# Kernel tuning notes

Measured on AMD Instinct MI355X. Metric: run time of the kernel, lower is better.

## Reference

```python
import jax, jax.numpy as jnp
import numpy as np
from jax import lax

B, S, D, N_ORDER, K = 8, 4096, 256, 2, 3
G = N_ORDER + 1  # groups in HyenaProjection
EPS_FILT = 1e-8


def setup_inputs() -> dict:
    key = jax.random.key(0)
    ks = jax.random.split(key, 8)
    sc = 0.02
    # positions: per-row arange with trailing -1 padding (one contiguous read per row)
    vl = jnp.where(jnp.arange(B) % 2 == 0, S, (3 * S) // 4)
    pos = jnp.where(jnp.arange(S, dtype=jnp.int32)[None, :] < vl[:, None],
                    jnp.arange(S, dtype=jnp.int32)[None, :], -1)
    return {
        "embeddings": jax.random.normal(ks[0], (B, S, D), jnp.float32),
        "positions": pos,
        "W_proj": jax.random.normal(ks[1], (D, G * D), jnp.float32) * sc,
        "conv_w": jax.random.normal(ks[2], (G * D, D, K), jnp.float32) * sc,
        "conv_b": jnp.zeros((G * D,), jnp.float32),
        "W1": jax.random.normal(ks[3], (D, D), jnp.float32) * sc,
        "b1": jnp.zeros((D,), jnp.float32),
        "ln_g": jnp.ones((D,), jnp.float32),
        "ln_b": jnp.zeros((D,), jnp.float32),
        "W2": jax.random.normal(ks[4], (D, N_ORDER * D), jnp.float32) * sc,
        "b2": jnp.zeros((N_ORDER * D,), jnp.float32),
        "ff_scale": jnp.ones((1, 1, N_ORDER * D), jnp.float32),
        "W_out": jax.random.normal(ks[5], (D, D), jnp.float32) * sc,
        "b_out": jnp.zeros((D,), jnp.float32),
    }


def adjust_positions(pos):
    pf = jnp.where(pos == -1, jnp.inf, pos.astype(jnp.float32))
    minp = pf.min(axis=-1, keepdims=True)
    adj = pos.astype(jnp.float32) - minp
    return jnp.where(pos == -1, -1.0, adj)


def rope_rotate(x, adj_pos):
    # compute_theta_vector + compute_rotation_angles + apply_dimensionwise_rotation
    d2 = x.shape[-1] // 2
    theta = 1.0 / (10000.0 ** (jnp.arange(d2, dtype=jnp.float32) / d2))
    ang = adj_pos[..., None] * theta  # (b, s, d/2)
    cos, sin = jnp.cos(ang), jnp.sin(ang)
    x1, x2 = x[..., 0::2], x[..., 1::2]
    r1 = x1 * cos - x2 * sin
    r2 = x1 * sin + x2 * cos
    return jnp.stack([r1, r2], axis=-1).reshape(x.shape)


def feed_forward(x, W1, b1, ln_g, ln_b, W2, b2, ff_scale):
    h = x @ W1 + b1
    mu = h.mean(-1, keepdims=True)
    var = ((h - mu) ** 2).mean(-1, keepdims=True)
    h = (h - mu) / jnp.sqrt(var + 1e-5) * ln_g + ln_b
    h = jax.nn.gelu(h, approximate=False)
    return (h @ W2 + b2) * ff_scale


def fft_long_conv(x, f, mask):
    # x, f: (b, d, s); 2L zero-padded circular conv == linear conv; torch norm='forward' pair => /n net
    L = x.shape[-1]
    n = 2 * L
    y = jnp.fft.irfft(jnp.fft.rfft(x, n=n) * jnp.fft.rfft(f, n=n), n=n)[..., :L] / n
    return y * mask[:, None, :]


def reference(embeddings, positions, W_proj, conv_w, conv_b, W1, b1, ln_g, ln_b, W2, b2, ff_scale, W_out, b_out):
    mask = (positions != -1).astype(embeddings.dtype)  # (b, s)

    # HyenaProjection: linear -> grouped short conv -> mask -> split into G streams
    z = jnp.einsum('bsd,de->bes', embeddings, W_proj)  # (b, G*d, s)
    z = lax.conv_general_dilated(z, conv_w, (1,), [(K // 2, K // 2)],
                                 dimension_numbers=('NCH', 'OIH', 'NCH'),
                                 feature_group_count=G)
    z = (z + conv_b[None, :, None]) * mask[:, None, :]
    zs = jnp.split(z, G, axis=1)  # G tensors of (b, d, s)

    # HyenaFilter: RoPE -> FFN -> reshape (b, n, d, s) -> L1 normalize over d
    t = rope_rotate(embeddings, adjust_positions(positions))
    h_hat = feed_forward(t, W1, b1, ln_g, ln_b, W2, b2, ff_scale)  # (b, s, n*d)
    h_hat = h_hat.reshape(h_hat.shape[0], h_hat.shape[1], N_ORDER, D).transpose(0, 2, 3, 1)
    h_hat = h_hat / (jnp.sum(jnp.abs(h_hat), axis=2, keepdims=True) + EPS_FILT)

    # Hyena recurrence with FFT long convolutions
    v = zs[-1]
    for i in range(N_ORDER):
        v = zs[i] * fft_long_conv(v, h_hat[:, i], mask)

    out = jnp.einsum('bds,de->bse', v, W_out) + b_out
    return out * mask[..., None]  # reassemble leaves padded positions zero
```

## Files before the change

### kernel.cpp

```cpp
#include <hip/hip_runtime.h>
#include <cstdint>

#define S_LEN 4096
#define D_DIM 256

#define OFF_MINP 0
#define OFF_WPT  16
#define OFF_WTH  (OFF_WPT + 768*256)
#define OFF_WTL  (OFF_WTH + 294912)
#define OFF_C    (OFF_WTL + 294912)
#define OFF_HH   (OFF_C + 8*768*4096)
#define OFF_V    (OFF_HH + 8*2*256*4096)
#define OFF_U    (OFF_V + 8*256*4096)


typedef __attribute__((ext_vector_type(8))) short short8;
typedef __attribute__((ext_vector_type(4))) float f32x4;

__device__ __forceinline__ unsigned int f2bf(float x) {
    union { float f; unsigned int u; } v; v.f = x;
    unsigned int r = v.u + 0x7fffu + ((v.u >> 16) & 1u);
    return r >> 16;
}
__device__ __forceinline__ float bf2f(unsigned int h) {
    union { unsigned int u; float f; } v; v.u = h << 16; return v.f;
}

__global__ __launch_bounds__(256) void k_minpos(const int* __restrict__ pos, float* __restrict__ minp)
{
    const int b = blockIdx.x;
    const int tid = threadIdx.x;
    int mn = 0x7fffffff;
    const int* p = pos + (size_t)b * S_LEN;
    for (int s = tid; s < S_LEN; s += 256) {
        const int v = p[s];
        if (v != -1) mn = min(mn, v);
    }
    __shared__ int red[256];
    red[tid] = mn;
    __syncthreads();
    for (int st = 128; st > 0; st >>= 1) {
        if (tid < st) red[tid] = min(red[tid], red[tid + st]);
        __syncthreads();
    }
    if (tid == 0) minp[b] = (float)red[0];
}

__global__ __launch_bounds__(256) void k_wpt(const float* __restrict__ Wp, float* __restrict__ WpT)
{
    __shared__ float t[32][33];
    const int e0 = blockIdx.x * 32;
    const int d0 = blockIdx.y * 32;
    const int lx = threadIdx.x & 31, ly = threadIdx.x >> 5;
#pragma unroll
    for (int q = 0; q < 4; ++q)
        t[ly + 8*q][lx] = Wp[(size_t)(d0 + ly + 8*q) * 768 + e0 + lx];
    __syncthreads();
#pragma unroll
    for (int q = 0; q < 4; ++q)
        WpT[(size_t)(e0 + ly + 8*q) * 256 + d0 + lx] = t[lx][ly + 8*q];
}

__global__ __launch_bounds__(256) void k_tsplit(const float* __restrict__ W, const int K, const int N,
                                                unsigned short* __restrict__ oh, unsigned short* __restrict__ ol)
{
    __shared__ float t[32][33];
    const int n0 = blockIdx.x * 32;
    const int k0 = blockIdx.y * 32;
    const int lx = threadIdx.x & 31, ly = threadIdx.x >> 5;
#pragma unroll
    for (int q = 0; q < 4; ++q)
        t[ly + 8*q][lx] = W[(size_t)(k0 + ly + 8*q) * N + n0 + lx];
    __syncthreads();
#pragma unroll
    for (int q = 0; q < 4; ++q) {
        const float v = t[lx][ly + 8*q];
        const unsigned int h = f2bf(v);
        oh[(size_t)(n0 + ly + 8*q) * K + k0 + lx] = (unsigned short)h;
        ol[(size_t)(n0 + ly + 8*q) * K + k0 + lx] = (unsigned short)f2bf(v - bf2f(h));
    }
}

__global__ __launch_bounds__(256) void k_weff(const float* __restrict__ WpT, const float* __restrict__ cw,
                                              unsigned short* __restrict__ wth, unsigned short* __restrict__ wtl)
{
    const int o = blockIdx.x;
    const int d = threadIdx.x;
    const int g = o >> 8;
    __shared__ float cwrow[768];
    for (int i = threadIdx.x; i < 768; i += 256) cwrow[i] = cw[(size_t)o * 768 + i];
    __syncthreads();
    float a0 = 0.f, a1 = 0.f, a2 = 0.f;
    const float* wb = WpT + (size_t)(g * 256) * 256 + d;
#pragma unroll 4
    for (int i = 0; i < 256; ++i) {
        const float wv = wb[(size_t)i * 256];
        a0 += wv * cwrow[i*3+0];
        a1 += wv * cwrow[i*3+1];
        a2 += wv * cwrow[i*3+2];
    }
    const float av[3] = {a0, a1, a2};
#pragma unroll
    for (int t = 0; t < 3; ++t) {
        const unsigned int hb = f2bf(av[t]);
        const unsigned int lb = f2bf(av[t] - bf2f(hb));
        wth[(size_t)o * 768 + t * 256 + d] = (unsigned short)hb;
        wtl[(size_t)o * 768 + t * 256 + d] = (unsigned short)lb;
    }
}

#define CG_LDA 40
__global__ __launch_bounds__(256, 3) void k_convgemm(
    const float* __restrict__ emb, const int* __restrict__ pos,
    const unsigned short* __restrict__ wth, const unsigned short* __restrict__ wtl,
    const float* __restrict__ convb, float* __restrict__ c)
{
    const int b  = blockIdx.z;
    const int o0 = blockIdx.y * 128;
    const int s0 = blockIdx.x * 128;
    const int tid  = threadIdx.x;
    const int wave = tid >> 6, lane = tid & 63;
    const int m16  = lane & 15, quad = lane >> 4;

    __shared__ __align__(16) unsigned short As[130 * CG_LDA];
    __shared__ __align__(16) unsigned short Bh[128 * CG_LDA];
    __shared__ __align__(16) unsigned short Bl[128 * CG_LDA];

    const int rA = tid >> 1;
    const int cA = (tid & 1) * 16;
    const int srowA = s0 + rA - 1;
    const bool vA = (srowA >= 0 && srowA < S_LEN);
    const float* embA = emb + ((size_t)b * S_LEN + (vA ? srowA : 0)) * D_DIM + cA;
    const int rT = 128 + (tid >> 3);
    const int cT = (tid & 7) * 4;
    const int srowT = s0 + rT - 1;
    const bool vT = (tid < 16) && (srowT >= 0 && srowT < S_LEN);
    const float* embT = emb + ((size_t)b * S_LEN + ((tid < 16 && vT) ? srowT : 0)) * D_DIM + cT;

    const int rB0 = tid >> 2,        gB0 = (tid & 3) * 8;
    const int rB1 = 64 + (tid >> 2), gB1 = gB0;

    float4 apf[4]; float4 apfT;
    uint4 bph0, bpl0, bph1, bpl1;

#pragma unroll
    for (int q = 0; q < 4; ++q) apf[q] = vA ? *(const float4*)(embA + q * 4) : make_float4(0.f,0.f,0.f,0.f);
    apfT = vT ? *(const float4*)(embT) : make_float4(0.f,0.f,0.f,0.f);
    {
        const size_t gi0 = (size_t)(o0 + rB0) * 768 + gB0;
        const size_t gi1 = (size_t)(o0 + rB1) * 768 + gB1;
        bph0 = *(const uint4*)(wth + gi0); bpl0 = *(const uint4*)(wtl + gi0);
        bph1 = *(const uint4*)(wth + gi1); bpl1 = *(const uint4*)(wtl + gi1);
    }

    f32x4 acc[2][8];
#pragma unroll
    for (int mt = 0; mt < 2; ++mt)
#pragma unroll
        for (int nt = 0; nt < 8; ++nt)
#pragma unroll
            for (int e = 0; e < 4; ++e) acc[mt][nt][e] = 0.f;

    for (int c8 = 0; c8 < 8; ++c8) {
        for (int t = 0; t < 3; ++t) {
            __syncthreads();
            if (t == 0) {
#pragma unroll
                for (int q = 0; q < 4; ++q) {
                    const float4 v = apf[q];
                    uint2 hp;
                    hp.x = f2bf(v.x) | (f2bf(v.y) << 16);
                    hp.y = f2bf(v.z) | (f2bf(v.w) << 16);
                    *(uint2*)&As[rA * CG_LDA + cA + q * 4] = hp;
                }
                if (tid < 16) {
                    const float4 v = apfT;
                    uint2 hp;
                    hp.x = f2bf(v.x) | (f2bf(v.y) << 16);
                    hp.y = f2bf(v.z) | (f2bf(v.w) << 16);
                    *(uint2*)&As[rT * CG_LDA + cT] = hp;
                }
                if (c8 < 7) {
                    const int base = (c8 + 1) * 32;
#pragma unroll
                    for (int q = 0; q < 4; ++q) apf[q] = vA ? *(const float4*)(embA + base + q * 4) : make_float4(0.f,0.f,0.f,0.f);
                    apfT = vT ? *(const float4*)(embT + base) : make_float4(0.f,0.f,0.f,0.f);
                }
            }
            *(uint4*)&Bh[rB0 * CG_LDA + gB0] = bph0;
            *(uint4*)&Bl[rB0 * CG_LDA + gB0] = bpl0;
            *(uint4*)&Bh[rB1 * CG_LDA + gB1] = bph1;
            *(uint4*)&Bl[rB1 * CG_LDA + gB1] = bpl1;
            if (!(c8 == 7 && t == 2)) {
                const int t2  = (t == 2) ? 0 : (t + 1);
                const int c82 = c8 + (t == 2);
                const int kbase = t2 * 256 + c82 * 32;
                const size_t gi0 = (size_t)(o0 + rB0) * 768 + kbase + gB0;
                const size_t gi1 = (size_t)(o0 + rB1) * 768 + kbase + gB1;
                bph0 = *(const uint4*)(wth + gi0); bpl0 = *(const uint4*)(wtl + gi0);
                bph1 = *(const uint4*)(wth + gi1); bpl1 = *(const uint4*)(wtl + gi1);
            }
            __syncthreads();
            short8 ah[2];
#pragma unroll
            for (int mt = 0; mt < 2; ++mt) {
                const int ar = (wave * 32 + mt * 16 + m16 + t) * CG_LDA + quad * 8;
                ah[mt] = *(const short8*)&As[ar];
            }
#pragma unroll
            for (int nt = 0; nt < 8; ++nt) {
                const int br = (nt * 16 + m16) * CG_LDA + quad * 8;
                const short8 bh = *(const short8*)&Bh[br];
                const short8 bl = *(const short8*)&Bl[br];
#pragma unroll
                for (int mt = 0; mt < 2; ++mt) {
                    acc[mt][nt] = __builtin_amdgcn_mfma_f32_16x16x32_bf16(ah[mt], bh, acc[mt][nt], 0, 0, 0);
                    acc[mt][nt] = __builtin_amdgcn_mfma_f32_16x16x32_bf16(ah[mt], bl, acc[mt][nt], 0, 0, 0);
                }
            }
        }
    }
    __syncthreads();

    float msk[2][4];
#pragma unroll
    for (int mt = 0; mt < 2; ++mt) {
        const int s = s0 + wave * 32 + mt * 16 + quad * 4;
        const int4 p4 = *(const int4*)(pos + (size_t)b * S_LEN + s);
        msk[mt][0] = (p4.x != -1) ? 1.f : 0.f;
        msk[mt][1] = (p4.y != -1) ? 1.f : 0.f;
        msk[mt][2] = (p4.z != -1) ? 1.f : 0.f;
        msk[mt][3] = (p4.w != -1) ? 1.f : 0.f;
    }
#pragma unroll
    for (int nt = 0; nt < 8; ++nt) {
        const int o = o0 + nt * 16 + m16;
        const float cb = convb[o];
#pragma unroll
        for (int mt = 0; mt < 2; ++mt) {
            const int s = s0 + wave * 32 + mt * 16 + quad * 4;
            float4 r;
            r.x = (acc[mt][nt][0] + cb) * msk[mt][0];
            r.y = (acc[mt][nt][1] + cb) * msk[mt][1];
            r.z = (acc[mt][nt][2] + cb) * msk[mt][2];
            r.w = (acc[mt][nt][3] + cb) * msk[mt][3];
            *(float4*)(c + ((size_t)(b * 768 + o)) * S_LEN + s) = r;
        }
    }
}

#define FF_LDA 264
#define FF_LDB 136
__global__ __launch_bounds__(256, 2) void k_ff(
    const float* __restrict__ emb, const int* __restrict__ pos, const float* __restrict__ minp,
    const unsigned short* __restrict__ w1th, const unsigned short* __restrict__ w1tl,
    const float* __restrict__ b1,
    const float* __restrict__ lng, const float* __restrict__ lnb,
    const unsigned short* __restrict__ w2th, const unsigned short* __restrict__ w2tl,
    const float* __restrict__ b2, const float* __restrict__ ffs, float* __restrict__ hh)
{
    const int b   = blockIdx.y;
    const int s0  = blockIdx.x * 64;
    const int tid = threadIdx.x;
    const int wave = tid >> 6, lane = tid & 63;
    const int m16  = lane & 15, quad = lane >> 4;

    __shared__ __align__(16) unsigned short Th[64 * FF_LDA];
    __shared__ __align__(16) unsigned short Bsh[16 * FF_LDB];
    __shared__ __align__(16) unsigned short Bsl[16 * FF_LDB];
    __shared__ float th_s[128];

    if (tid < 128) th_s[tid] = expf(-(float)tid * 0.07195578415606394f);
    __syncthreads();

    {
        const int r    = tid >> 2;
        const int col0 = (tid & 3) * 64;
        const int s    = s0 + r;
        const int p    = pos[(size_t)b * S_LEN + s];
        const float adj = (p == -1) ? -1.f : ((float)p - minp[b]);
        const float* ep = emb + ((size_t)b * S_LEN + s) * D_DIM;
#pragma unroll
        for (int p8 = 0; p8 < 8; ++p8) {
            const int cbase = col0 + p8 * 8;
            const float4 va = *(const float4*)(ep + cbase);
            const float4 vb4 = *(const float4*)(ep + cbase + 4);
            const float x[8] = {va.x, va.y, va.z, va.w, vb4.x, vb4.y, vb4.z, vb4.w};
            unsigned int uh[4];
#pragma unroll
            for (int jj = 0; jj < 4; ++jj) {
                const int j = (cbase >> 1) + jj;
                const float theta = th_s[j];
                float sn, cs;
                sincosf(adj * theta, &sn, &cs);
                const float x1 = x[2*jj], x2 = x[2*jj+1];
                const float r1 = x1 * cs - x2 * sn;
                const float r2 = x1 * sn + x2 * cs;
                uh[jj] = f2bf(r1) | (f2bf(r2) << 16);
            }
            uint4 wh;
            wh.x = uh[0]; wh.y = uh[1]; wh.z = uh[2]; wh.w = uh[3];
            *(uint4*)&Th[r * FF_LDA + cbase] = wh;
        }
    }
    __syncthreads();

    const int rowA  = wave * 16 + m16;
    const int strow = tid >> 4;
    const int stks  = (tid & 15) * 8;

    f32x4 acc1[16];
#pragma unroll
    for (int nt = 0; nt < 16; ++nt)
#pragma unroll
        for (int e = 0; e < 4; ++e) acc1[nt][e] = 0.f;

    uint4 pfh, pfl;
    {
        const size_t gi = (size_t)strow * 256 + stks;
        pfh = *(const uint4*)(w1th + gi);
        pfl = *(const uint4*)(w1tl + gi);
    }
    for (int kh = 0; kh < 2; ++kh) {
        short8 a1h[4];
#pragma unroll
        for (int c4 = 0; c4 < 4; ++c4) {
            const int ar = rowA * FF_LDA + kh * 128 + c4 * 32 + quad * 8;
            a1h[c4] = *(const short8*)&Th[ar];
        }
#pragma unroll
        for (int nt = 0; nt < 16; ++nt) {
            __syncthreads();
            *(uint4*)&Bsh[strow * FF_LDB + stks] = pfh;
            *(uint4*)&Bsl[strow * FF_LDB + stks] = pfl;
            if (!(kh == 1 && nt == 15)) {
                const int nt2 = (nt + 1) & 15;
                const int kh2 = kh + (nt == 15);
                const size_t gi = (size_t)(nt2 * 16 + strow) * 256 + kh2 * 128 + stks;
                pfh = *(const uint4*)(w1th + gi);
                pfl = *(const uint4*)(w1tl + gi);
            }
            __syncthreads();
#pragma unroll
            for (int c4 = 0; c4 < 4; ++c4) {
                const int br = m16 * FF_LDB + c4 * 32 + quad * 8;
                const short8 bh = *(const short8*)&Bsh[br];
                const short8 bl = *(const short8*)&Bsl[br];
                acc1[nt] = __builtin_amdgcn_mfma_f32_16x16x32_bf16(a1h[c4], bh, acc1[nt], 0, 0, 0);
                acc1[nt] = __builtin_amdgcn_mfma_f32_16x16x32_bf16(a1h[c4], bl, acc1[nt], 0, 0, 0);
            }
        }
    }

    float sume[4] = {0.f, 0.f, 0.f, 0.f}, sumq[4] = {0.f, 0.f, 0.f, 0.f};
#pragma unroll
    for (int nt = 0; nt < 16; ++nt) {
        const float bb = b1[nt * 16 + m16];
#pragma unroll
        for (int e = 0; e < 4; ++e) {
            const float v = acc1[nt][e] + bb;
            acc1[nt][e] = v;
            sume[e] += v;
            sumq[e] += v * v;
        }
    }
#pragma unroll
    for (int e = 0; e < 4; ++e) {
#pragma unroll
        for (int off = 1; off < 16; off <<= 1) {
            sume[e] += __shfl_xor(sume[e], off, 64);
            sumq[e] += __shfl_xor(sumq[e], off, 64);
        }
    }
    float mu[4], rs[4];
#pragma unroll
    for (int e = 0; e < 4; ++e) {
        mu[e] = sume[e] * (1.f / 256.f);
        const float var = sumq[e] * (1.f / 256.f) - mu[e] * mu[e];
        rs[e] = rsqrtf(var + 1e-5f);
    }

    {
        const size_t gi = (size_t)strow * 256 + stks;
        pfh = *(const uint4*)(w2th + gi);
        pfl = *(const uint4*)(w2tl + gi);
    }

    __syncthreads();
#pragma unroll
    for (int nt = 0; nt < 16; ++nt) {
        const int col = nt * 16 + m16;
        const float g  = lng[col];
        const float be = lnb[col];
#pragma unroll
        for (int e = 0; e < 4; ++e) {
            const float h  = (acc1[nt][e] - mu[e]) * rs[e] * g + be;
            const float hg = 0.5f * h * (1.f + erff(h * 0.7071067811865475f));
            const int li = (wave * 16 + quad * 4 + e) * FF_LDA + col;
            Th[li] = (unsigned short)f2bf(hg);
        }
    }
    __syncthreads();

    f32x4 acc2[32];
#pragma unroll
    for (int nt = 0; nt < 32; ++nt)
#pragma unroll
        for (int e = 0; e < 4; ++e) acc2[nt][e] = 0.f;

    for (int kh = 0; kh < 2; ++kh) {
        short8 a2h[4];
#pragma unroll
        for (int c4 = 0; c4 < 4; ++c4) {
            const int ar = rowA * FF_LDA + kh * 128 + c4 * 32 + quad * 8;
            a2h[c4] = *(const short8*)&Th[ar];
        }
#pragma unroll
        for (int nt = 0; nt < 32; ++nt) {
            __syncthreads();
            *(uint4*)&Bsh[strow * FF_LDB + stks] = pfh;
            *(uint4*)&Bsl[strow * FF_LDB + stks] = pfl;
            if (!(kh == 1 && nt == 31)) {
                const int nt2 = (nt + 1) & 31;
                const int kh2 = kh + (nt == 31);
                const size_t gi = (size_t)(nt2 * 16 + strow) * 256 + kh2 * 128 + stks;
                pfh = *(const uint4*)(w2th + gi);
                pfl = *(const uint4*)(w2tl + gi);
            }
            __syncthreads();
#pragma unroll
            for (int c4 = 0; c4 < 4; ++c4) {
                const int br = m16 * FF_LDB + c4 * 32 + quad * 8;
                const short8 bh = *(const short8*)&Bsh[br];
                const short8 bl = *(const short8*)&Bsl[br];
                acc2[nt] = __builtin_amdgcn_mfma_f32_16x16x32_bf16(a2h[c4], bh, acc2[nt], 0, 0, 0);
                acc2[nt] = __builtin_amdgcn_mfma_f32_16x16x32_bf16(a2h[c4], bl, acc2[nt], 0, 0, 0);
            }
        }
    }

    float sm[2][4] = {{0.f,0.f,0.f,0.f},{0.f,0.f,0.f,0.f}};
#pragma unroll
    for (int nt = 0; nt < 32; ++nt) {
        const int col = nt * 16 + m16;
        const float bb = b2[col];
        const float fs = ffs[col];
#pragma unroll
        for (int e = 0; e < 4; ++e) {
            const float v = (acc2[nt][e] + bb) * fs;
            acc2[nt][e] = v;
            sm[nt >> 4][e] += fabsf(v);
        }
    }
#pragma unroll
    for (int i = 0; i < 2; ++i)
#pragma unroll
        for (int e = 0; e < 4; ++e) {
#pragma unroll
            for (int off = 1; off < 16; off <<= 1)
                sm[i][e] += __shfl_xor(sm[i][e], off, 64);
        }
#pragma unroll
    for (int nt = 0; nt < 32; ++nt) {
        const int i = nt >> 4;
        const int d = (nt & 15) * 16 + m16;
        float4 o4;
        o4.x = acc2[nt][0] / (sm[i][0] + 1e-8f);
        o4.y = acc2[nt][1] / (sm[i][1] + 1e-8f);
        o4.z = acc2[nt][2] / (sm[i][2] + 1e-8f);
        o4.w = acc2[nt][3] / (sm[i][3] + 1e-8f);
        *(float4*)(hh + ((size_t)((b * 2 + i) * 256 + d)) * S_LEN + s0 + wave * 16 + quad * 4) = o4;
    }
}

#define XS_PAD   960
#define XS_ELEMS 5056
#define FRX_WORDS 4160
__device__ __forceinline__ int xsw(int blk) { return blk ^ ((blk >> 3) & 7); }

#define CONV_ACCUM_LOOP(ACC)                                                         \
    for (int i = 0; i < 32; ++i) {                                                   \
        const int r = 2 * i + wid;                                                   \
        const int ea_r = eA_base - 64 * r;                                           \
        short8 afr[4][2];                                                            \
        _Pragma("unroll")                                                            \
        for (int mt = 0; mt < 4; ++mt)                                               \
            _Pragma("unroll")                                                        \
            for (int kc = 0; kc < 2; ++kc) {                                         \
                const int e = ea_r - 16 * mt + 32 * kc;                              \
                union { unsigned int u[4]; short8 s; } cvt;                          \
                cvt.u[0] = frx[e];                                                   \
                cvt.u[1] = frx[e + 2];                                               \
                cvt.u[2] = frx[e + 4];                                               \
                cvt.u[3] = frx[e + 6];                                               \
                afr[mt][kc] = cvt.s;                                                 \
            }                                                                        \
        const int ptmin = r >> 4;                                                    \
        const int ob_r = oB_base - 64 * r;                                           \
        _Pragma("unroll")                                                            \
        for (int pt = 0; pt < 4; ++pt) {                                             \
            if (pt >= ptmin) {                                                       \
                const int o0 = ob_r + 1024 * pt;                                     \
                const short8 bfr0 = *(const short8*)(xs + xsw(o0 >> 3) * 8);         \
                const short8 bfr1 = *(const short8*)(xs + xsw((o0 + 32) >> 3) * 8);  \
                _Pragma("unroll")                                                    \
                for (int mt = 0; mt < 4; ++mt) {                                     \
                    ACC[mt][pt] = __builtin_amdgcn_mfma_f32_16x16x32_bf16(afr[mt][0], bfr0, ACC[mt][pt], 0, 0, 0); \
                    ACC[mt][pt] = __builtin_amdgcn_mfma_f32_16x16x32_bf16(afr[mt][1], bfr1, ACC[mt][pt], 0, 0, 0); \
                }                                                                    \
            }                                                                        \
        }                                                                            \
    }

__global__ __launch_bounds__(128) void k_conv2x(
    const float* __restrict__ cbuf, const float* __restrict__ hh,
    float* __restrict__ outb)
{
    const int d = blockIdx.x;
    const int b = blockIdx.y;
    const int tid  = threadIdx.x;
    const int lane = tid & 63;
    const int wid  = tid >> 6;
    const float* xp  = cbuf + ((size_t)(b * 768 + 512 + d)) * S_LEN;
    const float* fp0 = hh   + ((size_t)((b * 2 + 0) * 256 + d)) * S_LEN;
    const float* fp1 = hh   + ((size_t)((b * 2 + 1) * 256 + d)) * S_LEN;
    const float* zp0 = cbuf + ((size_t)(b * 768 +   0 + d)) * S_LEN;
    const float* zp1 = cbuf + ((size_t)(b * 768 + 256 + d)) * S_LEN;
    float* op = outb + ((size_t)(b * 256 + d)) * S_LEN;

    __shared__ __align__(16) unsigned short xs[XS_ELEMS];
    __shared__ __align__(16) unsigned int   frx[FRX_WORDS];

    float4 f1pf[8];
#pragma unroll
    for (int it = 0; it < 8; ++it)
        f1pf[it] = *(const float4*)(fp1 + (it * 128 + tid) * 4);

    {
        for (int blk = tid; blk < 120; blk += 128) {
            int4 z; z.x = 0; z.y = 0; z.z = 0; z.w = 0;
            *(int4*)(xs + xsw(blk) * 8) = z;
        }
#pragma unroll
        for (int it = 0; it < 4; ++it) {
            const int idx = it * 128 + tid;
            const int j = idx * 8;
            const float4 v0 = *(const float4*)(xp + j);
            const float4 v1 = *(const float4*)(xp + j + 4);
            int4 w;
            w.x = (int)(f2bf(v0.x) | (f2bf(v0.y) << 16));
            w.y = (int)(f2bf(v0.z) | (f2bf(v0.w) << 16));
            w.z = (int)(f2bf(v1.x) | (f2bf(v1.y) << 16));
            w.w = (int)(f2bf(v1.z) | (f2bf(v1.w) << 16));
            *(int4*)(xs + xsw(120 + idx) * 8) = w;
        }
    }
    {
        if (tid < 64) frx[4096 + tid] = 0u;
        if (tid == 0) frx[4095] = f2bf(fp0[0]);
#pragma unroll
        for (int it = 0; it < 8; ++it) {
            const int j = (it * 128 + tid) * 4;
            const float4 v = *(const float4*)(fp0 + j);
            const float f4 = (j + 4 < S_LEN) ? fp0[j + 4] : 0.f;
            frx[4094 - j] = f2bf(v.y) | (f2bf(v.x) << 16);
            frx[4093 - j] = f2bf(v.z) | (f2bf(v.y) << 16);
            frx[4092 - j] = f2bf(v.w) | (f2bf(v.z) << 16);
            if (j < 4092) frx[4091 - j] = f2bf(f4) | (f2bf(v.w) << 16);
        }
    }
    __syncthreads();

    const int m    = lane & 15;
    const int quad = lane >> 4;
    const int eA_base = 4095 - m + quad * 8;
    const int oB_base = XS_PAD + 64 * m + quad * 8;
    const float inv = 1.f / 8192.f;
    float* red = (float*)frx;

    f32x4 acc[4][4];
#pragma unroll
    for (int mt = 0; mt < 4; ++mt)
#pragma unroll
        for (int pt = 0; pt < 4; ++pt)
#pragma unroll
            for (int e = 0; e < 4; ++e) acc[mt][pt][e] = 0.f;

    CONV_ACCUM_LOOP(acc)

    __syncthreads();
    if (wid == 1) {
#pragma unroll
        for (int mt = 0; mt < 4; ++mt)
#pragma unroll
            for (int pt = 0; pt < 4; ++pt)
                *(f32x4*)&red[((mt * 4 + pt) * 64 + lane) * 4] = acc[mt][pt];
    }
    __syncthreads();
    if (wid == 0) {
#pragma unroll
        for (int mt = 0; mt < 4; ++mt)
#pragma unroll
            for (int pt = 0; pt < 4; ++pt) {
                const f32x4 po = *(const f32x4*)&red[((mt * 4 + pt) * 64 + lane) * 4];
                const int p  = 16 * pt + m;
                const int sv = 64 * p + 16 * mt + quad * 4;
                const float4 z4 = *(const float4*)(zp0 + sv);
                const float v0 = z4.x * (acc[mt][pt][0] + po[0]) * inv;
                const float v1 = z4.y * (acc[mt][pt][1] + po[1]) * inv;
                const float v2 = z4.z * (acc[mt][pt][2] + po[2]) * inv;
                const float v3 = z4.w * (acc[mt][pt][3] + po[3]) * inv;
                uint2 hp;
                hp.x = f2bf(v0) | (f2bf(v1) << 16);
                hp.y = f2bf(v2) | (f2bf(v3) << 16);
                *(uint2*)(xs + xsw(120 + (sv >> 3)) * 8 + (sv & 7)) = hp;
            }
    }
    __syncthreads();

    {
        if (tid < 64) frx[4096 + tid] = 0u;
        if (tid == 0) frx[4095] = f2bf(fp1[0]);
#pragma unroll
        for (int it = 0; it < 8; ++it) {
            const int j = (it * 128 + tid) * 4;
            const float4 v = f1pf[it];
            const float f4 = (j + 4 < S_LEN) ? fp1[j + 4] : 0.f;
            frx[4094 - j] = f2bf(v.y) | (f2bf(v.x) << 16);
            frx[4093 - j] = f2bf(v.z) | (f2bf(v.y) << 16);
            frx[4092 - j] = f2bf(v.w) | (f2bf(v.z) << 16);
            if (j < 4092) frx[4091 - j] = f2bf(f4) | (f2bf(v.w) << 16);
        }
    }
#pragma unroll
    for (int mt = 0; mt < 4; ++mt)
#pragma unroll
        for (int pt = 0; pt < 4; ++pt)
#pragma unroll
            for (int e = 0; e < 4; ++e) acc[mt][pt][e] = 0.f;
    __syncthreads();

    CONV_ACCUM_LOOP(acc)

    __syncthreads();
    if (wid == 1) {
#pragma unroll
        for (int mt = 0; mt < 4; ++mt)
#pragma unroll
            for (int pt = 0; pt < 4; ++pt)
                *(f32x4*)&red[((mt * 4 + pt) * 64 + lane) * 4] = acc[mt][pt];
    }
    __syncthreads();
    if (wid == 0) {
#pragma unroll
        for (int mt = 0; mt < 4; ++mt)
#pragma unroll
            for (int pt = 0; pt < 4; ++pt) {
                const f32x4 po = *(const f32x4*)&red[((mt * 4 + pt) * 64 + lane) * 4];
                const int p  = 16 * pt + m;
                const int sv = 64 * p + 16 * mt + quad * 4;
                const float4 z4 = *(const float4*)(zp1 + sv);
                float4 o4;
                o4.x = z4.x * (acc[mt][pt][0] + po[0]) * inv;
                o4.y = z4.y * (acc[mt][pt][1] + po[1]) * inv;
                o4.z = z4.z * (acc[mt][pt][2] + po[2]) * inv;
                o4.w = z4.w * (acc[mt][pt][3] + po[3]) * inv;
                *(float4*)(op + sv) = o4;
            }
    }
}

__global__ __launch_bounds__(256) void k_out(
    const float* __restrict__ v, const float* __restrict__ Wo,
    const float* __restrict__ bo, const int* __restrict__ pos,
    float* __restrict__ out)
{
    const int b   = blockIdx.y;
    const int s0  = blockIdx.x * 32;
    const int tid = threadIdx.x;
    __shared__ float vs[256 * 36];
    {
        const float4* src = (const float4*)(v + ((size_t)(b*256 + tid)) * S_LEN + s0);
#pragma unroll
        for (int q = 0; q < 8; ++q) {
            *(float4*)&vs[tid*36 + q*4] = src[q];
        }
    }
    __syncthreads();
    float acc[32];
#pragma unroll
    for (int r = 0; r < 32; ++r) acc[r] = 0.f;
    for (int dd = 0; dd < 256; ++dd) {
        const float w = Wo[(size_t)dd * 256 + tid];
        const float* vr = &vs[dd * 36];
#pragma unroll
        for (int q = 0; q < 8; ++q) {
            const float4 x4 = *(const float4*)&vr[q*4];
            acc[q*4+0] += x4.x * w;
            acc[q*4+1] += x4.y * w;
            acc[q*4+2] += x4.z * w;
            acc[q*4+3] += x4.w * w;
        }
    }
    const float bb = bo[tid];
#pragma unroll
    for (int r = 0; r < 32; ++r) {
        const int s = s0 + r;
        const float m = (pos[(size_t)b * S_LEN + s] != -1) ? 1.f : 0.f;
        out[((size_t)b * S_LEN + s) * 256 + tid] = (acc[r] + bb) * m;
    }
}

extern "C" void kernel_launch(void* const* d_in, const int* in_sizes, int n_in,
                              void* d_out, int out_size, void* d_ws, size_t ws_size,
                              hipStream_t stream) {
    const float* emb = (const float*)d_in[0];
    const int*   pos = (const int*)  d_in[1];
    const float* Wp  = (const float*)d_in[2];
    const float* cw  = (const float*)d_in[3];
    const float* cb  = (const float*)d_in[4];
    const float* W1  = (const float*)d_in[5];
    const float* b1  = (const float*)d_in[6];
    const float* lg  = (const float*)d_in[7];
    const float* lb  = (const float*)d_in[8];
    const float* W2  = (const float*)d_in[9];
    const float* b2  = (const float*)d_in[10];
    const float* ffs = (const float*)d_in[11];
    const float* Wo  = (const float*)d_in[12];
    const float* bo  = (const float*)d_in[13];

    float* ws   = (float*)d_ws;
    float* minp = ws + OFF_MINP;
    float* wpt  = ws + OFF_WPT;
    unsigned short* wth = (unsigned short*)(ws + OFF_WTH);
    unsigned short* wtl = (unsigned short*)(ws + OFF_WTL);
    float* c    = ws + OFF_C;
    float* hh   = ws + OFF_HH;
    float* vb   = ws + OFF_V;
    float* ub   = ws + OFF_U;

    unsigned short* w1th = (unsigned short*)vb;
    unsigned short* w1tl = w1th + 256 * 256;
    unsigned short* w2th = w1tl + 256 * 256;
    unsigned short* w2tl = w2th + 512 * 256;

    k_minpos<<<dim3(8), dim3(256), 0, stream>>>(pos, minp);
    k_wpt<<<dim3(24, 8), dim3(256), 0, stream>>>(Wp, wpt);
    k_weff<<<dim3(768), dim3(256), 0, stream>>>(wpt, cw, wth, wtl);
    k_tsplit<<<dim3(8, 8), dim3(256), 0, stream>>>(W1, 256, 256, w1th, w1tl);
    k_tsplit<<<dim3(16, 8), dim3(256), 0, stream>>>(W2, 256, 512, w2th, w2tl);
    k_convgemm<<<dim3(32, 6, 8), dim3(256), 0, stream>>>(emb, pos, wth, wtl, cb, c);
    k_ff<<<dim3(64, 8), dim3(256), 0, stream>>>(emb, pos, minp, w1th, w1tl, b1, lg, lb, w2th, w2tl, b2, ffs, hh);
    k_conv2x<<<dim3(256, 8), dim3(128), 0, stream>>>(c, hh, ub);
    k_out<<<dim3(128, 8), dim3(256), 0, stream>>>(ub, Wo, bo, pos, (float*)d_out);
}
```

Baseline: 484.0 us.

## Move output projection to bf16 split MFMA and widen conv filter LDS reads

```diff
diff --git a/kernel.cpp b/kernel.cpp
--- a/kernel.cpp
+++ b/kernel.cpp
@@ -488,11 +488,13 @@
             _Pragma("unroll")                                                        \
             for (int kc = 0; kc < 2; ++kc) {                                         \
                 const int e = ea_r - 16 * mt + 32 * kc;                              \
+                const uint2 d0 = frxd[e + 2];                                        \
+                const uint2 d1 = frxd[e + 6];                                        \
                 union { unsigned int u[4]; short8 s; } cvt;                          \
-                cvt.u[0] = frx[e];                                                   \
-                cvt.u[1] = frx[e + 2];                                               \
-                cvt.u[2] = frx[e + 4];                                               \
-                cvt.u[3] = frx[e + 6];                                               \
+                cvt.u[0] = d0.y;                                                     \
+                cvt.u[1] = d0.x;                                                     \
+                cvt.u[2] = d1.y;                                                     \
+                cvt.u[3] = d1.x;                                                     \
                 afr[mt][kc] = cvt.s;                                                 \
             }                                                                        \
         const int ptmin = r >> 4;                                                    \
@@ -512,6 +514,37 @@
         }                                                                            \
     }
 
+#define BUILD_FRXD(FPTR, VEXPR)                                                      \
+    {                                                                                \
+        _Pragma("unroll")                                                            \
+        for (int it = 0; it < 8; ++it) {                                             \
+            const int j = (it * 128 + tid) * 4;                                      \
+            const float4 v = (VEXPR);                                                \
+            const float4 g4 = (j + 4 < S_LEN) ? *(const float4*)((FPTR) + j + 4)     \
+                                              : make_float4(0.f,0.f,0.f,0.f);       \
+            const unsigned int w0 = f2bf(v.y)  | (f2bf(v.x)  << 16);                 \
+            const unsigned int w1 = f2bf(v.z)  | (f2bf(v.y)  << 16);                 \
+            const unsigned int w2 = f2bf(v.w)  | (f2bf(v.z)  << 16);                 \
+            const unsigned int w3 = f2bf(g4.x) | (f2bf(v.w)  << 16);                 \
+            const unsigned int w4 = f2bf(g4.y) | (f2bf(g4.x) << 16);                 \
+            const unsigned int w5 = f2bf(g4.z) | (f2bf(g4.y) << 16);                 \
+            frxd[4094 - j] = make_uint2(w0, w2);                                     \
+            frxd[4093 - j] = make_uint2(w1, w3);                                     \
+            frxd[4092 - j] = make_uint2(w2, w4);                                     \
+            if (j < 4092) frxd[4091 - j] = make_uint2(w3, w5);                       \
+        }                                                                            \
+        if (tid == 0) {                                                              \
+            const float4 v0 = *(const float4*)(FPTR);                                \
+            const unsigned int a95 = f2bf(v0.x);                                     \
+            const unsigned int w94 = f2bf(v0.y) | (f2bf(v0.x) << 16);                \
+            const unsigned int w93 = f2bf(v0.z) | (f2bf(v0.y) << 16);                \
+            frxd[4095] = make_uint2(a95, w93);                                       \
+            frxd[4096] = make_uint2(0u, w94);                                        \
+            frxd[4097] = make_uint2(0u, a95);                                        \
+        }                                                                            \
+        if (tid >= 2 && tid < 64) frxd[4096 + tid] = make_uint2(0u, 0u);             \
+    }
+
 __global__ __launch_bounds__(128) void k_conv2x(
     const float* __restrict__ cbuf, const float* __restrict__ hh,
     float* __restrict__ outb)
@@ -529,7 +562,7 @@
     float* op = outb + ((size_t)(b * 256 + d)) * S_LEN;
 
     __shared__ __align__(16) unsigned short xs[XS_ELEMS];
-    __shared__ __align__(16) unsigned int   frx[FRX_WORDS];
+    __shared__ __align__(16) uint2 frxd[FRX_WORDS];
 
     float4 f1pf[8];
 #pragma unroll
@@ -555,20 +588,7 @@
             *(int4*)(xs + xsw(120 + idx) * 8) = w;
         }
     }
-    {
-        if (tid < 64) frx[4096 + tid] = 0u;
-        if (tid == 0) frx[4095] = f2bf(fp0[0]);
-#pragma unroll
-        for (int it = 0; it < 8; ++it) {
-            const int j = (it * 128 + tid) * 4;
-            const float4 v = *(const float4*)(fp0 + j);
-            const float f4 = (j + 4 < S_LEN) ? fp0[j + 4] : 0.f;
-            frx[4094 - j] = f2bf(v.y) | (f2bf(v.x) << 16);
-            frx[4093 - j] = f2bf(v.z) | (f2bf(v.y) << 16);
-            frx[4092 - j] = f2bf(v.w) | (f2bf(v.z) << 16);
-            if (j < 4092) frx[4091 - j] = f2bf(f4) | (f2bf(v.w) << 16);
-        }
-    }
+    BUILD_FRXD(fp0, *(const float4*)(fp0 + j))
     __syncthreads();
 
     const int m    = lane & 15;
@@ -576,7 +596,7 @@
     const int eA_base = 4095 - m + quad * 8;
     const int oB_base = XS_PAD + 64 * m + quad * 8;
     const float inv = 1.f / 8192.f;
-    float* red = (float*)frx;
+    float* red = (float*)frxd;
 
     f32x4 acc[4][4];
 #pragma unroll
@@ -618,20 +638,7 @@
     }
     __syncthreads();
 
-    {
-        if (tid < 64) frx[4096 + tid] = 0u;
-        if (tid == 0) frx[4095] = f2bf(fp1[0]);
-#pragma unroll
-        for (int it = 0; it < 8; ++it) {
-            const int j = (it * 128 + tid) * 4;
-            const float4 v = f1pf[it];
-            const float f4 = (j + 4 < S_LEN) ? fp1[j + 4] : 0.f;
-            frx[4094 - j] = f2bf(v.y) | (f2bf(v.x) << 16);
-            frx[4093 - j] = f2bf(v.z) | (f2bf(v.y) << 16);
-            frx[4092 - j] = f2bf(v.w) | (f2bf(v.z) << 16);
-            if (j < 4092) frx[4091 - j] = f2bf(f4) | (f2bf(v.w) << 16);
-        }
-    }
+    BUILD_FRXD(fp1, f1pf[it])
 #pragma unroll
     for (int mt = 0; mt < 4; ++mt)
 #pragma unroll
@@ -670,44 +677,91 @@
     }
 }
 
-__global__ __launch_bounds__(256) void k_out(
-    const float* __restrict__ v, const float* __restrict__ Wo,
-    const float* __restrict__ bo, const int* __restrict__ pos,
-    float* __restrict__ out)
+__global__ __launch_bounds__(256, 2) void k_out(
+    const float* __restrict__ u, const unsigned short* __restrict__ woth,
+    const unsigned short* __restrict__ wotl, const float* __restrict__ bo,
+    const int* __restrict__ pos, float* __restrict__ out)
 {
     const int b   = blockIdx.y;
-    const int s0  = blockIdx.x * 32;
+    const int s0  = blockIdx.x * 64;
     const int tid = threadIdx.x;
-    __shared__ float vs[256 * 36];
+    const int wave = tid >> 6, lane = tid & 63;
+    const int m16  = lane & 15, quad = lane >> 4;
+
+    __shared__ __align__(16) unsigned short Bsh[16 * FF_LDB];
+    __shared__ __align__(16) unsigned short Bsl[16 * FF_LDB];
+
+    const int strow = tid >> 4;
+    const int stks  = (tid & 15) * 8;
+
+    const int sA = s0 + wave * 16 + m16;
+    const float* uA = u + (size_t)b * 256 * S_LEN + sA;
+
+    f32x4 acc[16];
+#pragma unroll
+    for (int nt = 0; nt < 16; ++nt)
+#pragma unroll
+        for (int e = 0; e < 4; ++e) acc[nt][e] = 0.f;
+
+    uint4 pfh, pfl;
     {
-        const float4* src = (const float4*)(v + ((size_t)(b*256 + tid)) * S_LEN + s0);
-#pragma unroll
-        for (int q = 0; q < 8; ++q) {
-            *(float4*)&vs[tid*36 + q*4] = src[q];
-        }
-    }
-    __syncthreads();
-    float acc[32];
-#pragma unroll
-    for (int r = 0; r < 32; ++r) acc[r] = 0.f;
-    for (int dd = 0; dd < 256; ++dd) {
-        const float w = Wo[(size_t)dd * 256 + tid];
-        const float* vr = &vs[dd * 36];
-#pragma unroll
-        for (int q = 0; q < 8; ++q) {
-            const float4 x4 = *(const float4*)&vr[q*4];
-            acc[q*4+0] += x4.x * w;
-            acc[q*4+1] += x4.y * w;
-            acc[q*4+2] += x4.z * w;
-            acc[q*4+3] += x4.w * w;
-        }
-    }
-    const float bb = bo[tid];
-#pragma unroll
-    for (int r = 0; r < 32; ++r) {
-        const int s = s0 + r;
-        const float m = (pos[(size_t)b * S_LEN + s] != -1) ? 1.f : 0.f;
-        out[((size_t)b * S_LEN + s) * 256 + tid] = (acc[r] + bb) * m;
+        const size_t gi = (size_t)strow * 256 + stks;
+        pfh = *(const uint4*)(woth + gi);
+        pfl = *(const uint4*)(wotl + gi);
+    }
+    for (int kh = 0; kh < 2; ++kh) {
+        short8 ah[4];
+#pragma unroll
+        for (int c4 = 0; c4 < 4; ++c4) {
+            const int k0 = kh * 128 + c4 * 32 + quad * 8;
+            float x[8];
+#pragma unroll
+            for (int j = 0; j < 8; ++j) x[j] = uA[(size_t)(k0 + j) * S_LEN];
+            union { unsigned int w[4]; short8 s; } pk;
+#pragma unroll
+            for (int j = 0; j < 4; ++j)
+                pk.w[j] = f2bf(x[2*j]) | (f2bf(x[2*j+1]) << 16);
+            ah[c4] = pk.s;
+        }
+#pragma unroll
+        for (int nt = 0; nt < 16; ++nt) {
+            __syncthreads();
+            *(uint4*)&Bsh[strow * FF_LDB + stks] = pfh;
+            *(uint4*)&Bsl[strow * FF_LDB + stks] = pfl;
+            if (!(kh == 1 && nt == 15)) {
+                const int nt2 = (nt + 1) & 15;
+                const int kh2 = kh + (nt == 15);
+                const size_t gi = (size_t)(nt2 * 16 + strow) * 256 + kh2 * 128 + stks;
+                pfh = *(const uint4*)(woth + gi);
+                pfl = *(const uint4*)(wotl + gi);
+            }
+            __syncthreads();
+#pragma unroll
+            for (int c4 = 0; c4 < 4; ++c4) {
+                const int br = m16 * FF_LDB + c4 * 32 + quad * 8;
+                const short8 bh = *(const short8*)&Bsh[br];
+                const short8 bl = *(const short8*)&Bsl[br];
+                acc[nt] = __builtin_amdgcn_mfma_f32_16x16x32_bf16(ah[c4], bh, acc[nt], 0, 0, 0);
+                acc[nt] = __builtin_amdgcn_mfma_f32_16x16x32_bf16(ah[c4], bl, acc[nt], 0, 0, 0);
+            }
+        }
+    }
+
+    const int sBase = s0 + wave * 16 + quad * 4;
+    const int4 p4 = *(const int4*)(pos + (size_t)b * S_LEN + sBase);
+    float msk[4];
+    msk[0] = (p4.x != -1) ? 1.f : 0.f;
+    msk[1] = (p4.y != -1) ? 1.f : 0.f;
+    msk[2] = (p4.z != -1) ? 1.f : 0.f;
+    msk[3] = (p4.w != -1) ? 1.f : 0.f;
+#pragma unroll
+    for (int nt = 0; nt < 16; ++nt) {
+        const int col = nt * 16 + m16;
+        const float bb = bo[col];
+#pragma unroll
+        for (int e = 0; e < 4; ++e) {
+            out[((size_t)b * S_LEN + sBase + e) * 256 + col] = (acc[nt][e] + bb) * msk[e];
+        }
     }
 }
 
@@ -743,14 +797,17 @@
     unsigned short* w1tl = w1th + 256 * 256;
     unsigned short* w2th = w1tl + 256 * 256;
     unsigned short* w2tl = w2th + 512 * 256;
+    unsigned short* woth = w2tl + 512 * 256;
+    unsigned short* wotl = woth + 256 * 256;
 
     k_minpos<<<dim3(8), dim3(256), 0, stream>>>(pos, minp);
     k_wpt<<<dim3(24, 8), dim3(256), 0, stream>>>(Wp, wpt);
     k_weff<<<dim3(768), dim3(256), 0, stream>>>(wpt, cw, wth, wtl);
     k_tsplit<<<dim3(8, 8), dim3(256), 0, stream>>>(W1, 256, 256, w1th, w1tl);
     k_tsplit<<<dim3(16, 8), dim3(256), 0, stream>>>(W2, 256, 512, w2th, w2tl);
+    k_tsplit<<<dim3(8, 8), dim3(256), 0, stream>>>(Wo, 256, 256, woth, wotl);
     k_convgemm<<<dim3(32, 6, 8), dim3(256), 0, stream>>>(emb, pos, wth, wtl, cb, c);
     k_ff<<<dim3(64, 8), dim3(256), 0, stream>>>(emb, pos, minp, w1th, w1tl, b1, lg, lb, w2th, w2tl, b2, ffs, hh);
     k_conv2x<<<dim3(256, 8), dim3(128), 0, stream>>>(c, hh, ub);
-    k_out<<<dim3(128, 8), dim3(256), 0, stream>>>(ub, Wo, bo, pos, (float*)d_out);
-}
+    k_out<<<dim3(64, 8), dim3(256), 0, stream>>>(ub, woth, wotl, bo, pos, (float*)d_out);
+}
```

New measurement: 466.7 us. -3.6%, faster.
